# Kernel optimization log

Hardware: AMD Instinct MI355X
Metric: run time of the kernel (lower is better)

Reference implementation:

```python
import jax, jax.numpy as jnp
import numpy as np

N = 50000      # nodes
E = 800000     # directed edges (before self loops)
IN = 64        # in_channels
HID = 96       # hidden_dim
HEADS = 4
C = HID // HEADS
L = 4          # num_layers
G = 1024       # num graphs (molecules)
OUT = 1
BN_EPS = 1e-5


def setup_inputs() -> dict:
    key = jax.random.key(0)
    ks = jax.random.split(key, 20)
    x = jax.random.normal(ks[0], (N, IN), jnp.float32)
    edge_index = jax.random.randint(ks[1], (2, E), 0, N, dtype=jnp.int32)
    batch = jnp.sort(jax.random.randint(ks[2], (N,), 0, G, dtype=jnp.int32))
    def lin(k, fi, fo):
        return jax.random.normal(k, (fi, fo), jnp.float32) / np.sqrt(fi)
    return {
        "x": x, "edge_index": edge_index, "batch": batch,
        "W_in": lin(ks[3], IN, HID), "b_in": jnp.zeros((HID,), jnp.float32),
        "Wg": jax.random.normal(ks[4], (L, HID, HID), jnp.float32) / np.sqrt(HID),
        "att_src": jax.random.normal(ks[5], (L, HEADS, C), jnp.float32) / np.sqrt(C),
        "att_dst": jax.random.normal(ks[6], (L, HEADS, C), jnp.float32) / np.sqrt(C),
        "bg": jnp.zeros((L, HID), jnp.float32),
        "gamma": jnp.ones((L, HID), jnp.float32),
        "beta": jnp.zeros((L, HID), jnp.float32),
        "rm": 0.1 * jax.random.normal(ks[7], (L, HID), jnp.float32),
        "rv": jax.random.uniform(ks[8], (L, HID), jnp.float32, 0.5, 1.5),
        "W_jk": lin(ks[9], HID * L, HID), "b_jk": jnp.zeros((HID,), jnp.float32),
        "W_h1": lin(ks[10], HID, HID), "b_h1": jnp.zeros((HID,), jnp.float32),
        "W_h2": lin(ks[11], HID, OUT), "b_h2": jnp.zeros((OUT,), jnp.float32),
    }


def gat_conv(h_in, src, dst, W, a_s, a_d, b):
    # PyG GATConv (concat=True, negative_slope=0.2), eval mode (no dropout)
    h = (h_in @ W).reshape(N, HEADS, C)                      # [N,H,C]
    e = (h * a_s).sum(-1)[src] + (h * a_d).sum(-1)[dst]      # [E',H]
    e = jax.nn.leaky_relu(e, 0.2)
    m = jax.ops.segment_max(e, dst, num_segments=N)          # segment softmax over dst
    p = jnp.exp(e - m[dst])
    z = jax.ops.segment_sum(p, dst, num_segments=N)
    alpha = p / (z[dst] + 1e-16)                             # [E',H]
    out = jax.ops.segment_sum(h[src] * alpha[:, :, None], dst, num_segments=N)
    return out.reshape(N, HID) + b


def reference(x, edge_index, batch, W_in, b_in, Wg, att_src, att_dst, bg,
              gamma, beta, rm, rv, W_jk, b_jk, W_h1, b_h1, W_h2, b_h2):
    # add self loops (PyG GATConv default)
    loops = jnp.arange(N, dtype=edge_index.dtype)
    src = jnp.concatenate([edge_index[0], loops])
    dst = jnp.concatenate([edge_index[1], loops])

    h = jax.nn.elu(x @ W_in + b_in)
    pooled = []
    for i in range(L):
        hn = gat_conv(h, src, dst, Wg[i], att_src[i], att_dst[i], bg[i])
        hn = (hn - rm[i]) / jnp.sqrt(rv[i] + BN_EPS) * gamma[i] + beta[i]
        h = h + jax.nn.elu(hn)                               # residual
        pooled.append(jax.ops.segment_sum(h, batch, num_segments=G))
    z = jax.nn.elu(jnp.concatenate(pooled, axis=-1) @ W_jk + b_jk)  # JK
    z = jax.nn.relu(z @ W_h1 + b_h1)
    return z @ W_h2 + b_h2                                    # [G, OUT]
```

## Files before the change

### kernel.cpp

```cpp
#include <hip/hip_runtime.h>
#include <hip/hip_bf16.h>
#include <math.h>

#define NODES 50000
#define EDGES 800000
#define EP    850000
#define INCH  64
#define HIDD  96
#define NHEAD 4
#define CHD   24
#define NLAY  4
#define NGRF  1024
#define BNEPS 1e-5f
#define NB    49

typedef short  bf16x8 __attribute__((ext_vector_type(8)));
typedef float  f32x4  __attribute__((ext_vector_type(4)));

__device__ __forceinline__ float elu1(float v) { return v > 0.f ? v : __expf(v) - 1.f; }

__device__ __forceinline__ unsigned short f2bf(float f) {
    unsigned u = __float_as_uint(f);
    return (unsigned short)((u + 0x7fffu + ((u >> 16) & 1u)) >> 16);
}

__device__ __forceinline__ float rl_f(float v, int l) {
    return __int_as_float(__builtin_amdgcn_readlane(__float_as_int(v), l));
}

__device__ __forceinline__ float bnorm(float a, const float* __restrict__ bg,
                                       const float* __restrict__ rm, const float* __restrict__ rv,
                                       const float* __restrict__ gamma, const float* __restrict__ beta,
                                       int ch) {
    float hn = a + bg[ch];
    return (hn - rm[ch]) / sqrtf(rv[ch] + BNEPS) * gamma[ch] + beta[ch];
}

__device__ __forceinline__ void edge_sd(int e, const int* __restrict__ S,
                                        const int* __restrict__ D, int& s, int& d) {
    if (e < EDGES) { s = S[e]; d = D[e]; } else { s = e - EDGES; d = s; }
}


__global__ __launch_bounds__(256) void k_count(const int* __restrict__ S, const int* __restrict__ D,
                                               int* __restrict__ cnt) {
    int e = blockIdx.x * blockDim.x + threadIdx.x;
    if (e >= EP) return;
    int s, d; edge_sd(e, S, D, s, d);
    atomicAdd(&cnt[d], 1);
}

__global__ __launch_bounds__(1024) void k_scan1(const int* __restrict__ cnt,
                                                int* __restrict__ off, int* __restrict__ bsum) {
    __shared__ int sd[1024];
    int t = threadIdx.x;
    int i = blockIdx.x * 1024 + t;
    int v = (i < NODES) ? cnt[i] : 0;
    sd[t] = v; __syncthreads();
    for (int o = 1; o < 1024; o <<= 1) {
        int tv = (t >= o) ? sd[t - o] : 0;
        __syncthreads();
        sd[t] += tv; __syncthreads();
    }
    if (i < NODES) off[i] = sd[t] - v;
    if (t == 1023) bsum[blockIdx.x] = sd[1023];
}

__global__ __launch_bounds__(1024) void k_scan3m(int* __restrict__ off, const int* __restrict__ bsum,
                                                 int* __restrict__ cursor) {
    int carry = 0;
    for (int b = 0; b < blockIdx.x; ++b) carry += bsum[b];
    int i = blockIdx.x * 1024 + threadIdx.x;
    if (i < NODES) {
        int o = off[i] + carry;
        off[i] = o;
        cursor[i] = o;
    }
    if (i == 0) off[NODES] = EP;
}

__global__ __launch_bounds__(256) void k_scatter(const int* __restrict__ S, const int* __restrict__ D,
                                                 int* __restrict__ cursor, int* __restrict__ csr_src) {
    int e = blockIdx.x * blockDim.x + threadIdx.x;
    if (e >= EP) return;
    int s, d; edge_sd(e, S, D, s, d);
    int pos = atomicAdd(&cursor[d], 1);
    csr_src[pos] = s;
}


__global__ __launch_bounds__(256) void k_in0(const float* __restrict__ x,
                                             const float* __restrict__ W_in,
                                             const float* __restrict__ b_in,
                                             const float* __restrict__ Wg0,
                                             const float* __restrict__ asrc,
                                             const float* __restrict__ adst,
                                             float* __restrict__ h,
                                             unsigned* __restrict__ hpb,
                                             float* __restrict__ as_,
                                             float* __restrict__ ad_,
                                             float* __restrict__ pooled_all) {
    __shared__ __align__(16) unsigned short WB[3 * 6 * 64 * 8];
    __shared__ float outT[4][16][97];
    int tid = threadIdx.x;
    int lane = tid & 63;
    int w = tid >> 6;

    for (size_t i = (size_t)blockIdx.x * 256 + tid; i < (size_t)NLAY * NGRF * HIDD;
         i += (size_t)gridDim.x * 256)
        pooled_all[i] = 0.f;

    for (int idx = tid; idx < INCH * HIDD; idx += 256) {
        int k = idx / HIDD, col = idx - k * HIDD;
        int kb = k >> 5, lg = (k & 31) >> 3, i = k & 7;
        int nt = col >> 4, cl = col & 15;
        WB[(((kb * 6) + nt) * 64 + (lg * 16 + cl)) * 8 + i] = f2bf(W_in[idx]);
    }
    __syncthreads();

    bf16x8 bf1[12];
#pragma unroll
    for (int f = 0; f < 12; ++f)
        bf1[f] = *(const bf16x8*)&WB[(f * 64 + lane) * 8];

    int nodeBase = blockIdx.x * 64 + w * 16;
    int arow = nodeBase + (lane & 15);
    int arowc = min(arow, NODES - 1);

    {
        f32x4 acc[6];
#pragma unroll
        for (int n = 0; n < 6; ++n) { acc[n][0]=0.f; acc[n][1]=0.f; acc[n][2]=0.f; acc[n][3]=0.f; }
#pragma unroll
        for (int kb = 0; kb < 2; ++kb) {
            const float* ap = x + (size_t)arowc * INCH + kb * 32 + (lane >> 4) * 8;
            float4 u0 = *(const float4*)ap;
            float4 u1 = *(const float4*)(ap + 4);
            bf16x8 af;
            af[0]=(short)f2bf(u0.x); af[1]=(short)f2bf(u0.y); af[2]=(short)f2bf(u0.z); af[3]=(short)f2bf(u0.w);
            af[4]=(short)f2bf(u1.x); af[5]=(short)f2bf(u1.y); af[6]=(short)f2bf(u1.z); af[7]=(short)f2bf(u1.w);
#pragma unroll
            for (int nt = 0; nt < 6; ++nt)
                acc[nt] = __builtin_amdgcn_mfma_f32_16x16x32_bf16(af, bf1[kb * 6 + nt], acc[nt], 0, 0, 0);
        }
#pragma unroll
        for (int nt = 0; nt < 6; ++nt) {
            int col = nt * 16 + (lane & 15);
            float b = b_in[col];
#pragma unroll
            for (int r = 0; r < 4; ++r)
                outT[w][(lane >> 4) * 4 + r][col] = elu1(acc[nt][r] + b);
        }
    }
    __syncthreads();

    for (int idx = tid; idx < HIDD * HIDD; idx += 256) {
        int k = idx / HIDD, col = idx - k * HIDD;
        int kb = k >> 5, lg = (k & 31) >> 3, i = k & 7;
        int nt = col >> 4, cl = col & 15;
        WB[(((kb * 6) + nt) * 64 + (lg * 16 + cl)) * 8 + i] = f2bf(Wg0[idx]);
    }
    __syncthreads();

    bf16x8 bf2[18];
#pragma unroll
    for (int f = 0; f < 18; ++f)
        bf2[f] = *(const bf16x8*)&WB[(f * 64 + lane) * 8];

    {
        int nl = lane >> 2, part = lane & 3;
        int noden = nodeBase + nl;
        if (noden < NODES) {
            float* hw = h + (size_t)noden * HIDD + part * 24;
            const float* row = &outT[w][nl][part * 24];
#pragma unroll
            for (int t = 0; t < 6; ++t)
                ((float4*)hw)[t] = *(const float4*)&row[t * 4];
        }
    }

    f32x4 acc2[6];
#pragma unroll
    for (int n = 0; n < 6; ++n) { acc2[n][0]=0.f; acc2[n][1]=0.f; acc2[n][2]=0.f; acc2[n][3]=0.f; }
#pragma unroll
    for (int kb = 0; kb < 3; ++kb) {
        const float* ap = &outT[w][lane & 15][kb * 32 + (lane >> 4) * 8];
        bf16x8 af;
#pragma unroll
        for (int i = 0; i < 8; ++i) af[i] = (short)f2bf(ap[i]);
#pragma unroll
        for (int nt = 0; nt < 6; ++nt)
            acc2[nt] = __builtin_amdgcn_mfma_f32_16x16x32_bf16(af, bf2[kb * 6 + nt], acc2[nt], 0, 0, 0);
    }
#pragma unroll
    for (int nt = 0; nt < 6; ++nt)
#pragma unroll
        for (int r = 0; r < 4; ++r)
            outT[w][(lane >> 4) * 4 + r][nt * 16 + (lane & 15)] = acc2[nt][r];

    int nl = lane >> 2, head = lane & 3;
    int node = nodeBase + nl;
    if (node < NODES) {
        const float* row = &outT[w][nl][head * CHD];
        unsigned* orow = hpb + (size_t)node * (HIDD / 2) + head * (CHD / 2);
#pragma unroll
        for (int t = 0; t < CHD / 2; ++t)
            orow[t] = (unsigned)f2bf(row[2 * t]) | ((unsigned)f2bf(row[2 * t + 1]) << 16);
        const float* s = asrc + head * CHD;
        const float* d = adst + head * CHD;
        float sa = 0.f, da = 0.f;
#pragma unroll
        for (int j = 0; j < CHD; ++j) { sa = fmaf(row[j], s[j], sa); da = fmaf(row[j], d[j], da); }
        as_[node * NHEAD + head] = sa;
        ad_[node * NHEAD + head] = da;
    }
}


__global__ __launch_bounds__(256) void k_proj(const float* __restrict__ h,
                                              const float* __restrict__ W,
                                              const float* __restrict__ asrc,
                                              const float* __restrict__ adst,
                                              unsigned* __restrict__ hpb,
                                              float* __restrict__ as_,
                                              float* __restrict__ ad_) {
    __shared__ __align__(16) unsigned short WB[3 * 6 * 64 * 8];
    __shared__ float outT[4][16][97];
    int tid = threadIdx.x;
    int lane = tid & 63;
    int w = tid >> 6;

    for (int idx = tid; idx < HIDD * HIDD; idx += 256) {
        int k = idx / HIDD, col = idx - k * HIDD;
        int kb = k >> 5, lg = (k & 31) >> 3, i = k & 7;
        int nt = col >> 4, cl = col & 15;
        WB[(((kb * 6) + nt) * 64 + (lg * 16 + cl)) * 8 + i] = f2bf(W[idx]);
    }
    __syncthreads();

    bf16x8 bfrag[18];
#pragma unroll
    for (int f = 0; f < 18; ++f)
        bfrag[f] = *(const bf16x8*)&WB[(f * 64 + lane) * 8];

    int nodeBase = blockIdx.x * 64 + w * 16;
    int arow = nodeBase + (lane & 15);
    int arowc = min(arow, NODES - 1);

    f32x4 acc[6];
#pragma unroll
    for (int n = 0; n < 6; ++n) { acc[n][0]=0.f; acc[n][1]=0.f; acc[n][2]=0.f; acc[n][3]=0.f; }

#pragma unroll
    for (int kb = 0; kb < 3; ++kb) {
        const float* ap = h + (size_t)arowc * HIDD + kb * 32 + (lane >> 4) * 8;
        float4 u0 = *(const float4*)ap;
        float4 u1 = *(const float4*)(ap + 4);
        bf16x8 af;
        af[0]=(short)f2bf(u0.x); af[1]=(short)f2bf(u0.y); af[2]=(short)f2bf(u0.z); af[3]=(short)f2bf(u0.w);
        af[4]=(short)f2bf(u1.x); af[5]=(short)f2bf(u1.y); af[6]=(short)f2bf(u1.z); af[7]=(short)f2bf(u1.w);
#pragma unroll
        for (int nt = 0; nt < 6; ++nt)
            acc[nt] = __builtin_amdgcn_mfma_f32_16x16x32_bf16(af, bfrag[kb * 6 + nt], acc[nt], 0, 0, 0);
    }

#pragma unroll
    for (int nt = 0; nt < 6; ++nt)
#pragma unroll
        for (int r = 0; r < 4; ++r)
            outT[w][(lane >> 4) * 4 + r][nt * 16 + (lane & 15)] = acc[nt][r];

    int nl = lane >> 2, head = lane & 3;
    int node = nodeBase + nl;
    if (node < NODES) {
        const float* row = &outT[w][nl][head * CHD];
        unsigned* orow = hpb + (size_t)node * (HIDD / 2) + head * (CHD / 2);
#pragma unroll
        for (int t = 0; t < CHD / 2; ++t)
            orow[t] = (unsigned)f2bf(row[2 * t]) | ((unsigned)f2bf(row[2 * t + 1]) << 16);
        const float* s = asrc + head * CHD;
        const float* d = adst + head * CHD;
        float sa = 0.f, da = 0.f;
#pragma unroll
        for (int j = 0; j < CHD; ++j) { sa = fmaf(row[j], s[j], sa); da = fmaf(row[j], d[j], da); }
        as_[node * NHEAD + head] = sa;
        ad_[node * NHEAD + head] = da;
    }
}


__global__ __launch_bounds__(256) void k_edge(const int* __restrict__ off,
                                              const int* __restrict__ csr,
                                              const float* __restrict__ as_,
                                              const float* __restrict__ ad_,
                                              const unsigned* __restrict__ hpb,
                                              const float* __restrict__ bg,
                                              const float* __restrict__ gamma,
                                              const float* __restrict__ beta,
                                              const float* __restrict__ rm,
                                              const float* __restrict__ rv,
                                              float* __restrict__ h,
                                              const int* __restrict__ batch,
                                              float* __restrict__ pooled) {
    __shared__ float plds[512];
    int tid = threadIdx.x;
    int lane = tid & 63;
    int n0 = __builtin_amdgcn_readfirstlane(blockIdx.x * 8 + (tid >> 6) * 2);
    int n1 = n0 + 1;
    int beg0 = off[n0], end0 = off[n0 + 1], end1 = off[n0 + 2];
    int beg1 = end0;

    int hd = lane & 3, slot = lane >> 2;
    float adv0 = ad_[n0 * NHEAD + hd];
    float adv1 = ad_[n1 * NHEAD + hd];
    const int hh = (lane < 48) ? (lane / 12) : 0;
    const bool gl = (lane < 48);
    const int wb = (tid & 192) * 2;

    float a00 = 0.f, a01 = 0.f, a10 = 0.f, a11 = 0.f, zA = 0.f, zB = 0.f;
    int ca = beg0, cb = beg1;
    int sA = 0, sB = 0;
    float evA = 0.f, evB = 0.f;
    if (ca < end0) { sA = csr[min(ca + slot, end0 - 1)]; evA = as_[sA * NHEAD + hd]; }
    if (cb < end1) { sB = csr[min(cb + slot, end1 - 1)]; evB = as_[sB * NHEAD + hd]; }

    while (ca < end0 || cb < end1) {
        int cntA = min(16, end0 - ca);
        int cntB = min(16, end1 - cb);
        if (cntA > 0) {
            float ev = evA + adv0;
            ev = ev > 0.f ? ev : 0.2f * ev;
            float p = (ca + slot < end0) ? __expf(ev) : 0.f;
            zA += p;
            plds[wb + lane] = p;
        }
        if (cntB > 0) {
            float ev = evB + adv1;
            ev = ev > 0.f ? ev : 0.2f * ev;
            float p = (cb + slot < end1) ? __expf(ev) : 0.f;
            zB += p;
            plds[wb + 64 + lane] = p;
        }
        int na = ca + (cntA > 0 ? 16 : 0);
        int nb = cb + (cntB > 0 ? 16 : 0);
        int sA2 = 0, sB2 = 0;
        float evA2 = 0.f, evB2 = 0.f;
        if (na < end0) { sA2 = csr[min(na + slot, end0 - 1)]; evA2 = as_[sA2 * NHEAD + hd]; }
        if (nb < end1) { sB2 = csr[min(nb + slot, end1 - 1)]; evB2 = as_[sB2 * NHEAD + hd]; }
        if (cntA > 0) {
#pragma unroll
            for (int j = 0; j < 16; ++j) {
                if (j < cntA) {
                    int sv = __builtin_amdgcn_readlane(sA, j * 4);
                    float al = plds[wb + j * 4 + hh];
                    if (gl) {
                        unsigned u = (hpb + (size_t)sv * (HIDD / 2))[lane];
                        a00 = fmaf(__uint_as_float(u << 16),         al, a00);
                        a01 = fmaf(__uint_as_float(u & 0xffff0000u), al, a01);
                    }
                }
            }
        }
        if (cntB > 0) {
#pragma unroll
            for (int j = 0; j < 16; ++j) {
                if (j < cntB) {
                    int sv = __builtin_amdgcn_readlane(sB, j * 4);
                    float al = plds[wb + 64 + j * 4 + hh];
                    if (gl) {
                        unsigned u = (hpb + (size_t)sv * (HIDD / 2))[lane];
                        a10 = fmaf(__uint_as_float(u << 16),         al, a10);
                        a11 = fmaf(__uint_as_float(u & 0xffff0000u), al, a11);
                    }
                }
            }
        }
        ca = na; cb = nb;
        sA = sA2; evA = evA2; sB = sB2; evB = evB2;
    }
#pragma unroll
    for (int o = 4; o < 64; o <<= 1) { zA += __shfl_xor(zA, o); zB += __shfl_xor(zB, o); }
    float za0 = rl_f(zA, 0), za1 = rl_f(zA, 1), za2 = rl_f(zA, 2), za3 = rl_f(zA, 3);
    float zb0 = rl_f(zB, 0), zb1 = rl_f(zB, 1), zb2 = rl_f(zB, 2), zb3 = rl_f(zB, 3);
    float zAl = (hh & 1) ? za1 : za0, zAh = (hh & 1) ? za3 : za2;
    float zBl = (hh & 1) ? zb1 : zb0, zBh = (hh & 1) ? zb3 : zb2;
    float zhA = (hh & 2) ? zAh : zAl;
    float zhB = (hh & 2) ? zBh : zBl;

    int g0 = batch[n0], g1 = batch[n1];
    if (gl) {
        float izA = 1.f / zhA, izB = 1.f / zhB;
        a00 *= izA; a01 *= izA; a10 *= izB; a11 *= izB;
        int ch0 = 2 * lane, ch1 = ch0 + 1;
        float hn00 = bnorm(a00, bg, rm, rv, gamma, beta, ch0);
        float hn01 = bnorm(a01, bg, rm, rv, gamma, beta, ch1);
        float hn10 = bnorm(a10, bg, rm, rv, gamma, beta, ch0);
        float hn11 = bnorm(a11, bg, rm, rv, gamma, beta, ch1);
        float2 hv0 = *(float2*)(h + (size_t)n0 * HIDD + ch0);
        float2 hv1 = *(float2*)(h + (size_t)n1 * HIDD + ch0);
        hv0.x += elu1(hn00); hv0.y += elu1(hn01);
        hv1.x += elu1(hn10); hv1.y += elu1(hn11);
        *(float2*)(h + (size_t)n0 * HIDD + ch0) = hv0;
        *(float2*)(h + (size_t)n1 * HIDD + ch0) = hv1;
        if (g0 == g1) {
            atomicAdd(&pooled[g0 * HIDD + ch0], hv0.x + hv1.x);
            atomicAdd(&pooled[g0 * HIDD + ch1], hv0.y + hv1.y);
        } else {
            atomicAdd(&pooled[g0 * HIDD + ch0], hv0.x);
            atomicAdd(&pooled[g0 * HIDD + ch1], hv0.y);
            atomicAdd(&pooled[g1 * HIDD + ch0], hv1.x);
            atomicAdd(&pooled[g1 * HIDD + ch1], hv1.y);
        }
    }
}


__global__ __launch_bounds__(128) void k_head(const float* __restrict__ pooled,
                                              const float* __restrict__ Wjk, const float* __restrict__ bjk,
                                              const float* __restrict__ Wh1, const float* __restrict__ bh1,
                                              const float* __restrict__ Wh2, const float* __restrict__ bh2,
                                              float* __restrict__ out) {
    __shared__ float pin[NLAY * HIDD];
    __shared__ float z1[HIDD];
    __shared__ float z2[HIDD];
    int g = blockIdx.x, tid = threadIdx.x;
    for (int idx = tid; idx < NLAY * HIDD; idx += blockDim.x) {
        int l = idx / HIDD, c = idx % HIDD;
        pin[idx] = pooled[(size_t)l * NGRF * HIDD + (size_t)g * HIDD + c];
    }
    __syncthreads();
    for (int c = tid; c < HIDD; c += blockDim.x) {
        float a = bjk[c];
#pragma unroll 8
        for (int k = 0; k < NLAY * HIDD; ++k) a = fmaf(pin[k], Wjk[k * HIDD + c], a);
        z1[c] = elu1(a);
    }
    __syncthreads();
    for (int c = tid; c < HIDD; c += blockDim.x) {
        float a = bh1[c];
#pragma unroll 8
        for (int k = 0; k < HIDD; ++k) a = fmaf(z1[k], Wh1[k * HIDD + c], a);
        z2[c] = fmaxf(a, 0.f);
    }
    __syncthreads();
    if (tid < 64) {
        float a = 0.f;
        for (int k = tid; k < HIDD; k += 64) a = fmaf(z2[k], Wh2[k], a);
#pragma unroll
        for (int o = 32; o > 0; o >>= 1) a += __shfl_down(a, o);
        if (tid == 0) out[g] = a + bh2[0];
    }
}

extern "C" void kernel_launch(void* const* d_in, const int* in_sizes, int n_in,
                              void* d_out, int out_size, void* d_ws, size_t ws_size,
                              hipStream_t stream) {
    const float* x     = (const float*)d_in[0];
    const int*   ei    = (const int*)d_in[1];
    const int*   batch = (const int*)d_in[2];
    const float* W_in  = (const float*)d_in[3];
    const float* b_in  = (const float*)d_in[4];
    const float* Wg    = (const float*)d_in[5];
    const float* att_s = (const float*)d_in[6];
    const float* att_d = (const float*)d_in[7];
    const float* bg    = (const float*)d_in[8];
    const float* gamma = (const float*)d_in[9];
    const float* beta  = (const float*)d_in[10];
    const float* rm    = (const float*)d_in[11];
    const float* rv    = (const float*)d_in[12];
    const float* Wjk   = (const float*)d_in[13];
    const float* bjk   = (const float*)d_in[14];
    const float* Wh1   = (const float*)d_in[15];
    const float* bh1   = (const float*)d_in[16];
    const float* Wh2   = (const float*)d_in[17];
    const float* bh2   = (const float*)d_in[18];
    float* out = (float*)d_out;

    const int* S = ei;
    const int* Dd = ei + EDGES;

    float* ws = (float*)d_ws;
    float*    h      = ws;
    float*    as_    = h    + (size_t)NODES * HIDD;
    float*    ad_    = as_  + (size_t)NODES * NHEAD;
    float*    pooled = ad_  + (size_t)NODES * NHEAD;
    unsigned* hpb    = (unsigned*)(pooled + (size_t)NLAY * NGRF * HIDD);
    int*      off    = (int*)(hpb + (size_t)NODES * (HIDD / 2));
    int*      cursor = off    + NODES + 2;
    int*      csr    = cursor + NODES;
    int*      cnt    = csr    + EP;
    int*      bsum   = cnt    + NODES;

    hipMemsetAsync(cnt, 0, sizeof(int) * NODES, stream);

    const int TB = 256;
    int gE    = (EP + TB - 1) / TB;
    int gTile = (NODES + 63) / 64;
    int gEdge = NODES / 8;

    k_count<<<gE, TB, 0, stream>>>(S, Dd, cnt);
    k_scan1<<<NB, 1024, 0, stream>>>(cnt, off, bsum);
    k_scan3m<<<NB, 1024, 0, stream>>>(off, bsum, cursor);
    k_scatter<<<gE, TB, 0, stream>>>(S, Dd, cursor, csr);

    k_in0<<<gTile, TB, 0, stream>>>(x, W_in, b_in, Wg, att_s, att_d,
                                    h, hpb, as_, ad_, pooled);
    k_edge<<<gEdge, TB, 0, stream>>>(off, csr, as_, ad_, hpb,
                                     bg, gamma, beta, rm, rv, h, batch, pooled);

    for (int i = 1; i < NLAY; ++i) {
        k_proj<<<gTile, TB, 0, stream>>>(h, Wg + (size_t)i * HIDD * HIDD,
                                         att_s + i * NHEAD * CHD, att_d + i * NHEAD * CHD,
                                         hpb, as_, ad_);
        k_edge<<<gEdge, TB, 0, stream>>>(off, csr, as_, ad_, hpb,
                                         bg + i * HIDD, gamma + i * HIDD, beta + i * HIDD,
                                         rm + i * HIDD, rv + i * HIDD, h, batch,
                                         pooled + (size_t)i * NGRF * HIDD);
    }

    k_head<<<NGRF, 128, 0, stream>>>(pooled, Wjk, bjk, Wh1, bh1, Wh2, bh2, out);
}
```

Baseline: 455.5 us.

## Reduce pooling atomics via block-level segment reduction and sharded pooled buffers

Instead of each wave issuing per-node atomicAdds into the graph-pooled sum, each block stages its 8 nodes' updated features in shared memory. It merges consecutive nodes belonging to the same graph (batch is sorted) and issues one atomic per run per channel. The pooled buffer is also replicated into 4 shards selected by block index to spread contention, and the head kernel sums the shards. This adds a block barrier, shared-memory traffic and a larger pooled buffer to zero.

```diff
diff --git a/kernel.cpp b/kernel.cpp
--- a/kernel.cpp
+++ b/kernel.cpp
@@ -13,6 +13,7 @@
 #define NGRF  1024
 #define BNEPS 1e-5f
 #define NB    49
+#define NSH   4
 
 typedef short  bf16x8 __attribute__((ext_vector_type(8)));
 typedef float  f32x4  __attribute__((ext_vector_type(4)));
@@ -106,7 +107,7 @@
     int lane = tid & 63;
     int w = tid >> 6;
 
-    for (size_t i = (size_t)blockIdx.x * 256 + tid; i < (size_t)NLAY * NGRF * HIDD;
+    for (size_t i = (size_t)blockIdx.x * 256 + tid; i < (size_t)NLAY * NSH * NGRF * HIDD;
          i += (size_t)gridDim.x * 256)
         pooled_all[i] = 0.f;
 
@@ -303,9 +304,12 @@
                                               const int* __restrict__ batch,
                                               float* __restrict__ pooled) {
     __shared__ float plds[512];
+    __shared__ float blk[8][HIDD];
+    __shared__ int   gblk[8];
     int tid = threadIdx.x;
     int lane = tid & 63;
-    int n0 = __builtin_amdgcn_readfirstlane(blockIdx.x * 8 + (tid >> 6) * 2);
+    int w = tid >> 6;
+    int n0 = __builtin_amdgcn_readfirstlane(blockIdx.x * 8 + w * 2);
     int n1 = n0 + 1;
     int beg0 = off[n0], end0 = off[n0 + 1], end1 = off[n0 + 2];
     int beg1 = end0;
@@ -402,15 +406,23 @@
         hv1.x += elu1(hn10); hv1.y += elu1(hn11);
         *(float2*)(h + (size_t)n0 * HIDD + ch0) = hv0;
         *(float2*)(h + (size_t)n1 * HIDD + ch0) = hv1;
-        if (g0 == g1) {
-            atomicAdd(&pooled[g0 * HIDD + ch0], hv0.x + hv1.x);
-            atomicAdd(&pooled[g0 * HIDD + ch1], hv0.y + hv1.y);
-        } else {
-            atomicAdd(&pooled[g0 * HIDD + ch0], hv0.x);
-            atomicAdd(&pooled[g0 * HIDD + ch1], hv0.y);
-            atomicAdd(&pooled[g1 * HIDD + ch0], hv1.x);
-            atomicAdd(&pooled[g1 * HIDD + ch1], hv1.y);
-        }
+        blk[w * 2 + 0][ch0] = hv0.x; blk[w * 2 + 0][ch1] = hv0.y;
+        blk[w * 2 + 1][ch0] = hv1.x; blk[w * 2 + 1][ch1] = hv1.y;
+    }
+    if (lane == 0) { gblk[w * 2] = g0; gblk[w * 2 + 1] = g1; }
+    __syncthreads();
+
+    if (tid < HIDD) {
+        float* pooledS = pooled + (size_t)(blockIdx.x & (NSH - 1)) * NGRF * HIDD;
+        float acc = blk[0][tid];
+        int g = gblk[0];
+        for (int r = 1; r < 8; ++r) {
+            int gr = gblk[r];
+            float v = blk[r][tid];
+            if (gr == g) acc += v;
+            else { atomicAdd(&pooledS[g * HIDD + tid], acc); g = gr; acc = v; }
+        }
+        atomicAdd(&pooledS[g * HIDD + tid], acc);
     }
 }
 
@@ -426,7 +438,11 @@
     int g = blockIdx.x, tid = threadIdx.x;
     for (int idx = tid; idx < NLAY * HIDD; idx += blockDim.x) {
         int l = idx / HIDD, c = idx % HIDD;
-        pin[idx] = pooled[(size_t)l * NGRF * HIDD + (size_t)g * HIDD + c];
+        float a = 0.f;
+#pragma unroll
+        for (int s = 0; s < NSH; ++s)
+            a += pooled[(((size_t)l * NSH + s) * NGRF + g) * HIDD + c];
+        pin[idx] = a;
     }
     __syncthreads();
     for (int c = tid; c < HIDD; c += blockDim.x) {
@@ -484,7 +500,7 @@
     float*    as_    = h    + (size_t)NODES * HIDD;
     float*    ad_    = as_  + (size_t)NODES * NHEAD;
     float*    pooled = ad_  + (size_t)NODES * NHEAD;
-    unsigned* hpb    = (unsigned*)(pooled + (size_t)NLAY * NGRF * HIDD);
+    unsigned* hpb    = (unsigned*)(pooled + (size_t)NLAY * NSH * NGRF * HIDD);
     int*      off    = (int*)(hpb + (size_t)NODES * (HIDD / 2));
     int*      cursor = off    + NODES + 2;
     int*      csr    = cursor + NODES;
@@ -515,7 +531,7 @@
         k_edge<<<gEdge, TB, 0, stream>>>(off, csr, as_, ad_, hpb,
                                          bg + i * HIDD, gamma + i * HIDD, beta + i * HIDD,
                                          rm + i * HIDD, rv + i * HIDD, h, batch,
-                                         pooled + (size_t)i * NGRF * HIDD);
+                                         pooled + (size_t)i * NSH * NGRF * HIDD);
     }
 
     k_head<<<NGRF, 128, 0, stream>>>(pooled, Wjk, bjk, Wh1, bh1, Wh2, bh2, out);
```

Measured after the change: 468.2 us. 1.03x slower.
